# Kernel optimization log

Hardware: AMD Instinct MI355X
Metric: run time of the kernel (lower is better)

Reference implementation:

```python
import jax, jax.numpy as jnp
import numpy as np

D = 512
H_MAX = 32
W_MAX = 32
BATCH = 16


def _embeds_1d(L: int, d: int) -> jnp.ndarray:
    # Faithful to torch _embeds_1d: denom = L ** (2*cumsum(ones)/d) = L**(2*(j+1)/d)
    # (numer broadcast interpreted as per-position arange over rows, the intended math)
    numer = jnp.arange(L, dtype=jnp.float32)[:, None]            # [L,1]
    exps = 2.0 * jnp.arange(1, d + 1, dtype=jnp.float32) / d     # [d]
    denom = jnp.float32(L) ** exps                               # [d]
    e = numer / denom                                            # [L,d]
    return jnp.zeros_like(e).at[:, 0::2].set(jnp.sin(e[:, 0::2])).at[:, 1::2].set(jnp.cos(e[:, 1::2]))


def make_embed(H: int, W: int, d: int) -> jnp.ndarray:
    # [H,W,d] = embed_h[:,None,:] + embed_w[None,:,:]
    return _embeds_1d(H, d)[:, None, :] + _embeds_1d(W, d)[None, :, :]


def setup_inputs() -> dict:
    key = jax.random.key(0)
    k1, k2 = jax.random.split(key)
    q = jax.random.normal(k1, (BATCH, H_MAX, W_MAX, D), dtype=jnp.float32)
    k = jax.random.normal(k2, (BATCH, H_MAX, W_MAX, D), dtype=jnp.float32)
    embed = make_embed(H_MAX, W_MAX, D)
    return {"q": q, "k": k, "embed": embed}


def reference(q, k, embed):
    # content->position logits + position->(content+position) logits
    # q: [b,i,j,d], k: [b,k,l,d], embed: [i,j,d] (= q_embed = k_embed)
    logits = (jnp.einsum('bijd,kld->bijkl', q, embed)
              + jnp.einsum('ijd,bkld->bijkl', embed, k + embed))
    return logits  # [b,i,j,k,l]
```

## Files before the change

### kernel.cpp

```cpp
#include <hip/hip_runtime.h>
#include <stdint.h>

#define DD 512
#define NP 1024
#define NB 16

typedef __attribute__((ext_vector_type(8))) __bf16 bf16x8;
typedef __attribute__((ext_vector_type(4))) float f32x4;

__global__ __launch_bounds__(256) void thin_gemm(
    const float* __restrict__ q, const float* __restrict__ kin,
    const float* __restrict__ embed,
    float* __restrict__ qhw, float* __restrict__ khw)
{
    __shared__ __align__(16) unsigned short EHW[64 * 512];

    const int tid  = threadIdx.x;
    const int lane = tid & 63;
    const int wid  = tid >> 6;

    #pragma unroll
    for (int it = 0; it < 16; ++it) {
        int flat = it * 2048 + tid * 8;
        int row = flat >> 9, col = flat & 511;
        int srcrow = (row < 32) ? (row << 5) : (row - 32);
        const float* sp = embed + (size_t)srcrow * DD + col;
        float4 a = *(const float4*)sp;
        float4 c = *(const float4*)(sp + 4);
        if (row >= 32) {
            float4 z0 = *(const float4*)(embed + col);
            float4 z1 = *(const float4*)(embed + col + 4);
            a.x -= z0.x; a.y -= z0.y; a.z -= z0.z; a.w -= z0.w;
            c.x -= z1.x; c.y -= z1.y; c.z -= z1.z; c.w -= z1.w;
        }
        bf16x8 r;
        r[0] = (__bf16)a.x; r[1] = (__bf16)a.y; r[2] = (__bf16)a.z; r[3] = (__bf16)a.w;
        r[4] = (__bf16)c.x; r[5] = (__bf16)c.y; r[6] = (__bf16)c.z; r[7] = (__bf16)c.w;
        int byte = (col * 2) ^ ((row & 7) << 4);
        *(bf16x8*)((char*)EHW + row * 1024 + byte) = r;
    }
    __syncthreads();

    const int g2 = (blockIdx.x >= 256) ? 1 : 0;
    const int lr = lane & 15;
    const int kq = (lane >> 4) * 8;

    const float* srcA;
    const float* srcE = nullptr;
    if (!g2) {
        srcA = q + (size_t)(blockIdx.x * 64 + wid * 16 + lr) * DD;
    } else {
        int idx = blockIdx.x - 256;
        int b = idx >> 4, qt = idx & 15;
        int Qrow = qt * 64 + wid * 16 + lr;
        srcA = kin + ((size_t)b * NP + Qrow) * DD;
        srcE = embed + (size_t)Qrow * DD;
    }

    f32x4 acc[4];
    #pragma unroll
    for (int n = 0; n < 4; ++n) acc[n] = (f32x4)0.0f;

    #pragma unroll 4
    for (int kk = 0; kk < DD; kk += 32) {
        float4 a0 = *(const float4*)(srcA + kk + kq);
        float4 a1 = *(const float4*)(srcA + kk + kq + 4);
        if (g2) {
            float4 e0 = *(const float4*)(srcE + kk + kq);
            float4 e1 = *(const float4*)(srcE + kk + kq + 4);
            a0.x += e0.x; a0.y += e0.y; a0.z += e0.z; a0.w += e0.w;
            a1.x += e1.x; a1.y += e1.y; a1.z += e1.z; a1.w += e1.w;
        }
        bf16x8 sf;
        sf[0]=(__bf16)a0.x; sf[1]=(__bf16)a0.y; sf[2]=(__bf16)a0.z; sf[3]=(__bf16)a0.w;
        sf[4]=(__bf16)a1.x; sf[5]=(__bf16)a1.y; sf[6]=(__bf16)a1.z; sf[7]=(__bf16)a1.w;
        bf16x8 ef[4];
        #pragma unroll
        for (int n = 0; n < 4; ++n) {
            int row = n * 16 + lr;
            int byte = ((kk + kq) * 2) ^ ((row & 7) << 4);
            ef[n] = *(const bf16x8*)((const char*)EHW + row * 1024 + byte);
        }
        if (!g2) {
            #pragma unroll
            for (int n = 0; n < 4; ++n)
                acc[n] = __builtin_amdgcn_mfma_f32_16x16x32_bf16(sf, ef[n], acc[n], 0, 0, 0);
        } else {
            #pragma unroll
            for (int n = 0; n < 4; ++n)
                acc[n] = __builtin_amdgcn_mfma_f32_16x16x32_bf16(ef[n], sf, acc[n], 0, 0, 0);
        }
    }

    if (!g2) {
        float* o = qhw + (size_t)(blockIdx.x * 64 + wid * 16 + (lane >> 4) * 4) * 64;
        #pragma unroll
        for (int n = 0; n < 4; ++n)
            #pragma unroll
            for (int i = 0; i < 4; ++i)
                o[(size_t)i * 64 + n * 16 + lr] = acc[n][i];
    } else {
        int idx = blockIdx.x - 256;
        int b = idx >> 4, qt = idx & 15;
        float* o = khw + (size_t)b * 64 * NP + qt * 64 + wid * 16 + lr;
        #pragma unroll
        for (int n = 0; n < 4; ++n) {
            int m = n * 16 + (lane >> 4) * 4;
            #pragma unroll
            for (int i = 0; i < 4; ++i)
                o[(size_t)(m + i) * NP] = acc[n][i];
        }
    }
}

__global__ __launch_bounds__(256) void assemble(
    const float* __restrict__ qhw, const float* __restrict__ khw,
    float* __restrict__ out)
{
    __shared__ __align__(16) float kh[NP];
    __shared__ __align__(16) float qq[16 * 64];

    const int tid = threadIdx.x;
    const int b   = blockIdx.x >> 6;
    const int i   = (blockIdx.x >> 1) & 31;
    const int jh  = blockIdx.x & 1;

    ((float4*)kh)[tid] = ((const float4*)(khw + ((size_t)b * 64 + i) * NP))[tid];
    ((float4*)qq)[tid] =
        ((const float4*)(qhw + ((size_t)(b * NP + i * 32 + jh * 16)) * 64))[tid];
    __syncthreads();

    const int Q0 = tid * 4;
    const int kidx = Q0 >> 5;
    const int lidx = Q0 & 31;
    const float4 khv = *(const float4*)&kh[Q0];

    float* orow = out + ((size_t)(b * NP + i * 32 + jh * 16)) * NP + Q0;
    const float* kwbase = khw + ((size_t)b * 64 + 32 + jh * 16) * NP + Q0;

    #pragma unroll 4
    for (int jj = 0; jj < 16; ++jj) {
        float4 kw = *(const float4*)(kwbase + (size_t)jj * NP);
        float qh  = qq[jj * 64 + kidx];
        float4 qw = *(const float4*)&qq[jj * 64 + 32 + lidx];
        float4 v;
        v.x = khv.x + kw.x + qh + qw.x;
        v.y = khv.y + kw.y + qh + qw.y;
        v.z = khv.z + kw.z + qh + qw.z;
        v.w = khv.w + kw.w + qh + qw.w;
        *(float4*)(orow + (size_t)jj * NP) = v;
    }
}

extern "C" void kernel_launch(void* const* d_in, const int* in_sizes, int n_in,
                              void* d_out, int out_size, void* d_ws, size_t ws_size,
                              hipStream_t stream) {
    const float* q = (const float*)d_in[0];
    const float* k = (const float*)d_in[1];
    const float* e = (const float*)d_in[2];
    float* out = (float*)d_out;

    float* qhw = (float*)d_ws;
    float* khw = qhw + (size_t)NB * NP * 64;

    hipLaunchKernelGGL(thin_gemm, dim3(512), dim3(256), 0, stream, q, k, e, qhw, khw);
    hipLaunchKernelGGL(assemble, dim3(1024), dim3(256), 0, stream, qhw, khw, out);
}
```

Measured before the change: 50.62 us.

## Precompute bf16 embedding fragments once and split GEMM into smaller tiles

Moves the per-block conversion of the 64x512 rank embedding into bf16 LDS into a separate tiny prep kernel. That kernel writes the values to workspace in MFMA fragment order, which the GEMM then reads straight from global/L2. The GEMM grid doubles to 1024 blocks of 32 rows, with waves split across rows and the N dimension. This drops the 64KB LDS use, which should allow higher occupancy, and removes the redundant conversion done in every block. The cost is an extra kernel launch and reading embedding fragments from L2 instead of LDS.

```diff
diff --git a/kernel.cpp b/kernel.cpp
--- a/kernel.cpp
+++ b/kernel.cpp
@@ -8,108 +8,102 @@
 typedef __attribute__((ext_vector_type(8))) __bf16 bf16x8;
 typedef __attribute__((ext_vector_type(4))) float f32x4;
 
-__global__ __launch_bounds__(256) void thin_gemm(
+__global__ __launch_bounds__(256) void prep_ehwf(
+    const float* __restrict__ embed, unsigned short* __restrict__ ehwf)
+{
+    int g = blockIdx.x * 256 + threadIdx.x;
+    int c = g & 3;
+    int row = (g >> 2) & 63;
+    int ks = g >> 8;
+    int col = ks * 32 + c * 8;
+    int srcrow = (row < 32) ? (row << 5) : (row - 32);
+    const float* src = embed + (size_t)srcrow * DD + col;
+    float4 a = *(const float4*)src;
+    float4 d = *(const float4*)(src + 4);
+    if (row >= 32) {
+        float4 z0 = *(const float4*)(embed + col);
+        float4 z1 = *(const float4*)(embed + col + 4);
+        a.x -= z0.x; a.y -= z0.y; a.z -= z0.z; a.w -= z0.w;
+        d.x -= z1.x; d.y -= z1.y; d.z -= z1.z; d.w -= z1.w;
+    }
+    bf16x8 r;
+    r[0]=(__bf16)a.x; r[1]=(__bf16)a.y; r[2]=(__bf16)a.z; r[3]=(__bf16)a.w;
+    r[4]=(__bf16)d.x; r[5]=(__bf16)d.y; r[6]=(__bf16)d.z; r[7]=(__bf16)d.w;
+    *(bf16x8*)(ehwf + (size_t)g * 8) = r;
+}
+
+__global__ __launch_bounds__(256, 4) void rank_gemm(
     const float* __restrict__ q, const float* __restrict__ kin,
     const float* __restrict__ embed,
+    const unsigned short* __restrict__ ehwf,
     float* __restrict__ qhw, float* __restrict__ khw)
 {
-    __shared__ __align__(16) unsigned short EHW[64 * 512];
-
     const int tid  = threadIdx.x;
     const int lane = tid & 63;
     const int wid  = tid >> 6;
-
-    #pragma unroll
-    for (int it = 0; it < 16; ++it) {
-        int flat = it * 2048 + tid * 8;
-        int row = flat >> 9, col = flat & 511;
-        int srcrow = (row < 32) ? (row << 5) : (row - 32);
-        const float* sp = embed + (size_t)srcrow * DD + col;
-        float4 a = *(const float4*)sp;
-        float4 c = *(const float4*)(sp + 4);
-        if (row >= 32) {
-            float4 z0 = *(const float4*)(embed + col);
-            float4 z1 = *(const float4*)(embed + col + 4);
-            a.x -= z0.x; a.y -= z0.y; a.z -= z0.z; a.w -= z0.w;
-            c.x -= z1.x; c.y -= z1.y; c.z -= z1.z; c.w -= z1.w;
-        }
-        bf16x8 r;
-        r[0] = (__bf16)a.x; r[1] = (__bf16)a.y; r[2] = (__bf16)a.z; r[3] = (__bf16)a.w;
-        r[4] = (__bf16)c.x; r[5] = (__bf16)c.y; r[6] = (__bf16)c.z; r[7] = (__bf16)c.w;
-        int byte = (col * 2) ^ ((row & 7) << 4);
-        *(bf16x8*)((char*)EHW + row * 1024 + byte) = r;
-    }
-    __syncthreads();
-
-    const int g2 = (blockIdx.x >= 256) ? 1 : 0;
+    const int wa = wid >> 1;
+    const int wn = wid & 1;
     const int lr = lane & 15;
     const int kq = (lane >> 4) * 8;
 
+    const bool g2 = blockIdx.x >= 512;
     const float* srcA;
     const float* srcE = nullptr;
     if (!g2) {
-        srcA = q + (size_t)(blockIdx.x * 64 + wid * 16 + lr) * DD;
+        srcA = q + (size_t)(blockIdx.x * 32 + wa * 16 + lr) * DD + kq;
     } else {
-        int idx = blockIdx.x - 256;
-        int b = idx >> 4, qt = idx & 15;
-        int Qrow = qt * 64 + wid * 16 + lr;
-        srcA = kin + ((size_t)b * NP + Qrow) * DD;
-        srcE = embed + (size_t)Qrow * DD;
+        int gi = blockIdx.x - 512;
+        int b = gi >> 5, qt = gi & 31;
+        int Q = qt * 32 + wa * 16 + lr;
+        srcA = kin + ((size_t)b * NP + Q) * DD + kq;
+        srcE = embed + (size_t)Q * DD + kq;
     }
+    const unsigned short* tb =
+        ehwf + ((size_t)(wn * 32 + lr) * 4 + (lane >> 4)) * 8;
 
-    f32x4 acc[4];
-    #pragma unroll
-    for (int n = 0; n < 4; ++n) acc[n] = (f32x4)0.0f;
+    f32x4 acc0 = (f32x4)0.0f, acc1 = (f32x4)0.0f;
 
     #pragma unroll 4
-    for (int kk = 0; kk < DD; kk += 32) {
-        float4 a0 = *(const float4*)(srcA + kk + kq);
-        float4 a1 = *(const float4*)(srcA + kk + kq + 4);
+    for (int ks = 0; ks < 16; ++ks) {
+        float4 a0 = *(const float4*)(srcA + ks * 32);
+        float4 a1 = *(const float4*)(srcA + ks * 32 + 4);
         if (g2) {
-            float4 e0 = *(const float4*)(srcE + kk + kq);
-            float4 e1 = *(const float4*)(srcE + kk + kq + 4);
+            float4 e0 = *(const float4*)(srcE + ks * 32);
+            float4 e1 = *(const float4*)(srcE + ks * 32 + 4);
             a0.x += e0.x; a0.y += e0.y; a0.z += e0.z; a0.w += e0.w;
             a1.x += e1.x; a1.y += e1.y; a1.z += e1.z; a1.w += e1.w;
         }
         bf16x8 sf;
         sf[0]=(__bf16)a0.x; sf[1]=(__bf16)a0.y; sf[2]=(__bf16)a0.z; sf[3]=(__bf16)a0.w;
         sf[4]=(__bf16)a1.x; sf[5]=(__bf16)a1.y; sf[6]=(__bf16)a1.z; sf[7]=(__bf16)a1.w;
-        bf16x8 ef[4];
-        #pragma unroll
-        for (int n = 0; n < 4; ++n) {
-            int row = n * 16 + lr;
-            int byte = ((kk + kq) * 2) ^ ((row & 7) << 4);
-            ef[n] = *(const bf16x8*)((const char*)EHW + row * 1024 + byte);
-        }
+        bf16x8 ef0 = *(const bf16x8*)(tb + (size_t)ks * 2048);
+        bf16x8 ef1 = *(const bf16x8*)(tb + (size_t)ks * 2048 + 512);
         if (!g2) {
-            #pragma unroll
-            for (int n = 0; n < 4; ++n)
-                acc[n] = __builtin_amdgcn_mfma_f32_16x16x32_bf16(sf, ef[n], acc[n], 0, 0, 0);
+            acc0 = __builtin_amdgcn_mfma_f32_16x16x32_bf16(sf, ef0, acc0, 0, 0, 0);
+            acc1 = __builtin_amdgcn_mfma_f32_16x16x32_bf16(sf, ef1, acc1, 0, 0, 0);
         } else {
-            #pragma unroll
-            for (int n = 0; n < 4; ++n)
-                acc[n] = __builtin_amdgcn_mfma_f32_16x16x32_bf16(ef[n], sf, acc[n], 0, 0, 0);
+            acc0 = __builtin_amdgcn_mfma_f32_16x16x32_bf16(ef0, sf, acc0, 0, 0, 0);
+            acc1 = __builtin_amdgcn_mfma_f32_16x16x32_bf16(ef1, sf, acc1, 0, 0, 0);
         }
     }
 
     if (!g2) {
-        float* o = qhw + (size_t)(blockIdx.x * 64 + wid * 16 + (lane >> 4) * 4) * 64;
+        float* o = qhw + (size_t)(blockIdx.x * 32 + wa * 16 + (lane >> 4) * 4) * 64
+                       + wn * 32 + lr;
         #pragma unroll
-        for (int n = 0; n < 4; ++n)
-            #pragma unroll
-            for (int i = 0; i < 4; ++i)
-                o[(size_t)i * 64 + n * 16 + lr] = acc[n][i];
+        for (int i = 0; i < 4; ++i) o[(size_t)i * 64]      = acc0[i];
+        #pragma unroll
+        for (int i = 0; i < 4; ++i) o[(size_t)i * 64 + 16] = acc1[i];
     } else {
-        int idx = blockIdx.x - 256;
-        int b = idx >> 4, qt = idx & 15;
-        float* o = khw + (size_t)b * 64 * NP + qt * 64 + wid * 16 + lr;
+        int gi = blockIdx.x - 512;
+        int b = gi >> 5, qt = gi & 31;
+        int Q = qt * 32 + wa * 16 + lr;
+        float* o = khw + (size_t)b * 64 * NP + Q;
+        int m0 = wn * 32 + (lane >> 4) * 4;
         #pragma unroll
-        for (int n = 0; n < 4; ++n) {
-            int m = n * 16 + (lane >> 4) * 4;
-            #pragma unroll
-            for (int i = 0; i < 4; ++i)
-                o[(size_t)(m + i) * NP] = acc[n][i];
-        }
+        for (int i = 0; i < 4; ++i) o[(size_t)(m0 + i) * NP]      = acc0[i];
+        #pragma unroll
+        for (int i = 0; i < 4; ++i) o[(size_t)(m0 + 16 + i) * NP] = acc1[i];
     }
 }
 
@@ -162,7 +156,10 @@
 
     float* qhw = (float*)d_ws;
     float* khw = qhw + (size_t)NB * NP * 64;
+    unsigned short* ehwf = (unsigned short*)(khw + (size_t)NB * 64 * NP);
 
-    hipLaunchKernelGGL(thin_gemm, dim3(512), dim3(256), 0, stream, q, k, e, qhw, khw);
+    hipLaunchKernelGGL(prep_ehwf, dim3(16), dim3(256), 0, stream, e, ehwf);
+    hipLaunchKernelGGL(rank_gemm, dim3(1024), dim3(256), 0, stream,
+                       q, k, e, ehwf, qhw, khw);
     hipLaunchKernelGGL(assemble, dim3(1024), dim3(256), 0, stream, qhw, khw, out);
 }
```

Measured after the change: 66.94 us. 1.32x slower.

## Precompute bf16 embed table and embed Gram, split-K the thin GEMM

Applied to the files above, without the earlier changes.

Adds a prep kernel that builds the swizzled bf16 embed-basis table once and computes the embed-embed Gram matrix G. This removes the per-block table construction and the per-element embed addition on the k side. The thin GEMM is split into two K halves with twice the blocks and stages the table into LDS via global_load_lds. The assemble kernel sums the partial halves and adds G terms. This adds a third launch and extra partial-sum reads in assemble in exchange for less redundant table work and more parallelism in the GEMM.

```diff
diff --git a/kernel.cpp b/kernel.cpp
--- a/kernel.cpp
+++ b/kernel.cpp
@@ -8,80 +8,123 @@
 typedef __attribute__((ext_vector_type(8))) __bf16 bf16x8;
 typedef __attribute__((ext_vector_type(4))) float f32x4;
 
-__global__ __launch_bounds__(256) void thin_gemm(
+#define QHW_HALF 1048576
+#define KHW_HALF 1048576
+
+__device__ __forceinline__ bf16x8 cvt8(const float4& a, const float4& b) {
+    bf16x8 r;
+    r[0]=(__bf16)a.x; r[1]=(__bf16)a.y; r[2]=(__bf16)a.z; r[3]=(__bf16)a.w;
+    r[4]=(__bf16)b.x; r[5]=(__bf16)b.y; r[6]=(__bf16)b.z; r[7]=(__bf16)b.w;
+    return r;
+}
+
+__device__ __forceinline__ bf16x8 ehw_row(const float* __restrict__ embed, int r,
+                                          int col, const float4& z0, const float4& z1) {
+    int srcrow = (r < 32) ? (r << 5) : (r - 32);
+    const float* sp = embed + (size_t)srcrow * DD + col;
+    float4 a = *(const float4*)sp;
+    float4 b = *(const float4*)(sp + 4);
+    if (r >= 32) {
+        a.x -= z0.x; a.y -= z0.y; a.z -= z0.z; a.w -= z0.w;
+        b.x -= z1.x; b.y -= z1.y; b.z -= z1.z; b.w -= z1.w;
+    }
+    return cvt8(a, b);
+}
+
+__global__ __launch_bounds__(256) void prep(
+    const float* __restrict__ embed, unsigned short* __restrict__ tbl,
+    float* __restrict__ G)
+{
+    const int tid = threadIdx.x;
+    if (blockIdx.x < 16) {
+        int g = blockIdx.x * 256 + tid;
+        int row = g >> 6;
+        int c8  = (g & 63) * 8;
+        float4 z0 = *(const float4*)(embed + c8);
+        float4 z1 = *(const float4*)(embed + c8 + 4);
+        bf16x8 r = ehw_row(embed, row, c8, z0, z1);
+        int h  = c8 >> 8;
+        int cl = c8 & 255;
+        int byte = (cl * 2) ^ ((row & 7) << 4);
+        *(bf16x8*)((char*)tbl + h * 32768 + row * 512 + byte) = r;
+    } else {
+        const int lane = tid & 63, wid = tid >> 6;
+        const int lr = lane & 15, kq = (lane >> 4) * 8;
+        f32x4 acc[4];
+        #pragma unroll
+        for (int n = 0; n < 4; ++n) acc[n] = (f32x4)0.0f;
+        for (int ks = 0; ks < 16; ++ks) {
+            int col = ks * 32 + kq;
+            float4 z0 = *(const float4*)(embed + col);
+            float4 z1 = *(const float4*)(embed + col + 4);
+            bf16x8 af = ehw_row(embed, wid * 16 + lr, col, z0, z1);
+            #pragma unroll
+            for (int n = 0; n < 4; ++n) {
+                bf16x8 bf = ehw_row(embed, n * 16 + lr, col, z0, z1);
+                acc[n] = __builtin_amdgcn_mfma_f32_16x16x32_bf16(af, bf, acc[n], 0, 0, 0);
+            }
+        }
+        int row0 = wid * 16 + (lane >> 4) * 4;
+        #pragma unroll
+        for (int n = 0; n < 4; ++n)
+            #pragma unroll
+            for (int i = 0; i < 4; ++i)
+                G[(size_t)(row0 + i) * 64 + n * 16 + lr] = acc[n][i];
+    }
+}
+
+__device__ __forceinline__ void gload_lds16(const void* g, void* l) {
+    __builtin_amdgcn_global_load_lds(
+        (const __attribute__((address_space(1))) unsigned int*)g,
+        (__attribute__((address_space(3))) unsigned int*)l,
+        16, 0, 0);
+}
+
+__global__ __launch_bounds__(256) void rank_gemm(
     const float* __restrict__ q, const float* __restrict__ kin,
-    const float* __restrict__ embed,
+    const unsigned short* __restrict__ tbl,
     float* __restrict__ qhw, float* __restrict__ khw)
 {
-    __shared__ __align__(16) unsigned short EHW[64 * 512];
+    __shared__ __align__(16) unsigned short T[64 * 256];
 
     const int tid  = threadIdx.x;
     const int lane = tid & 63;
     const int wid  = tid >> 6;
-
-    #pragma unroll
-    for (int it = 0; it < 16; ++it) {
-        int flat = it * 2048 + tid * 8;
-        int row = flat >> 9, col = flat & 511;
-        int srcrow = (row < 32) ? (row << 5) : (row - 32);
-        const float* sp = embed + (size_t)srcrow * DD + col;
-        float4 a = *(const float4*)sp;
-        float4 c = *(const float4*)(sp + 4);
-        if (row >= 32) {
-            float4 z0 = *(const float4*)(embed + col);
-            float4 z1 = *(const float4*)(embed + col + 4);
-            a.x -= z0.x; a.y -= z0.y; a.z -= z0.z; a.w -= z0.w;
-            c.x -= z1.x; c.y -= z1.y; c.z -= z1.z; c.w -= z1.w;
-        }
-        bf16x8 r;
-        r[0] = (__bf16)a.x; r[1] = (__bf16)a.y; r[2] = (__bf16)a.z; r[3] = (__bf16)a.w;
-        r[4] = (__bf16)c.x; r[5] = (__bf16)c.y; r[6] = (__bf16)c.z; r[7] = (__bf16)c.w;
-        int byte = (col * 2) ^ ((row & 7) << 4);
-        *(bf16x8*)((char*)EHW + row * 1024 + byte) = r;
-    }
-    __syncthreads();
-
-    const int g2 = (blockIdx.x >= 256) ? 1 : 0;
+    const int gsel  = blockIdx.x >> 9;
+    const int khalf = (blockIdx.x >> 8) & 1;
+    const int tile  = blockIdx.x & 255;
     const int lr = lane & 15;
     const int kq = (lane >> 4) * 8;
 
-    const float* srcA;
-    const float* srcE = nullptr;
-    if (!g2) {
-        srcA = q + (size_t)(blockIdx.x * 64 + wid * 16 + lr) * DD;
-    } else {
-        int idx = blockIdx.x - 256;
-        int b = idx >> 4, qt = idx & 15;
-        int Qrow = qt * 64 + wid * 16 + lr;
-        srcA = kin + ((size_t)b * NP + Qrow) * DD;
-        srcE = embed + (size_t)Qrow * DD;
-    }
+    const char* src = (const char*)tbl + khalf * 32768;
+    #pragma unroll
+    for (int c = 0; c < 8; ++c) {
+        int off = wid * 8192 + c * 1024;
+        gload_lds16(src + off + lane * 16, (char*)T + off);
+    }
+
+    const int grow = tile * 64 + wid * 16 + lr;
+    const float* srcA = (gsel ? kin : q) + (size_t)grow * DD + khalf * 256 + kq;
 
     f32x4 acc[4];
     #pragma unroll
     for (int n = 0; n < 4; ++n) acc[n] = (f32x4)0.0f;
 
+    __syncthreads();
+
     #pragma unroll 4
-    for (int kk = 0; kk < DD; kk += 32) {
-        float4 a0 = *(const float4*)(srcA + kk + kq);
-        float4 a1 = *(const float4*)(srcA + kk + kq + 4);
-        if (g2) {
-            float4 e0 = *(const float4*)(srcE + kk + kq);
-            float4 e1 = *(const float4*)(srcE + kk + kq + 4);
-            a0.x += e0.x; a0.y += e0.y; a0.z += e0.z; a0.w += e0.w;
-            a1.x += e1.x; a1.y += e1.y; a1.z += e1.z; a1.w += e1.w;
-        }
-        bf16x8 sf;
-        sf[0]=(__bf16)a0.x; sf[1]=(__bf16)a0.y; sf[2]=(__bf16)a0.z; sf[3]=(__bf16)a0.w;
-        sf[4]=(__bf16)a1.x; sf[5]=(__bf16)a1.y; sf[6]=(__bf16)a1.z; sf[7]=(__bf16)a1.w;
+    for (int ks = 0; ks < 8; ++ks) {
+        float4 a0 = *(const float4*)(srcA + ks * 32);
+        float4 a1 = *(const float4*)(srcA + ks * 32 + 4);
+        bf16x8 sf = cvt8(a0, a1);
         bf16x8 ef[4];
         #pragma unroll
         for (int n = 0; n < 4; ++n) {
             int row = n * 16 + lr;
-            int byte = ((kk + kq) * 2) ^ ((row & 7) << 4);
-            ef[n] = *(const bf16x8*)((const char*)EHW + row * 1024 + byte);
+            int byte = ((ks * 32 + kq) * 2) ^ ((row & 7) << 4);
+            ef[n] = *(const bf16x8*)((const char*)T + row * 512 + byte);
         }
-        if (!g2) {
+        if (!gsel) {
             #pragma unroll
             for (int n = 0; n < 4; ++n)
                 acc[n] = __builtin_amdgcn_mfma_f32_16x16x32_bf16(sf, ef[n], acc[n], 0, 0, 0);
@@ -92,42 +135,59 @@
         }
     }
 
-    if (!g2) {
-        float* o = qhw + (size_t)(blockIdx.x * 64 + wid * 16 + (lane >> 4) * 4) * 64;
+    if (!gsel) {
+        float* o = qhw + (size_t)khalf * QHW_HALF
+                 + (size_t)(tile * 64 + wid * 16 + (lane >> 4) * 4) * 64 + lr;
         #pragma unroll
         for (int n = 0; n < 4; ++n)
             #pragma unroll
             for (int i = 0; i < 4; ++i)
-                o[(size_t)i * 64 + n * 16 + lr] = acc[n][i];
+                o[(size_t)i * 64 + n * 16] = acc[n][i];
     } else {
-        int idx = blockIdx.x - 256;
-        int b = idx >> 4, qt = idx & 15;
-        float* o = khw + (size_t)b * 64 * NP + qt * 64 + wid * 16 + lr;
-        #pragma unroll
-        for (int n = 0; n < 4; ++n) {
-            int m = n * 16 + (lane >> 4) * 4;
+        int b = grow >> 10, Q = grow & 1023;
+        float* o = khw + (size_t)khalf * KHW_HALF + (size_t)b * 65536 + Q;
+        int m0 = (lane >> 4) * 4;
+        #pragma unroll
+        for (int n = 0; n < 4; ++n)
             #pragma unroll
             for (int i = 0; i < 4; ++i)
-                o[(size_t)(m + i) * NP] = acc[n][i];
-        }
+                o[(size_t)(n * 16 + m0 + i) * 1024] = acc[n][i];
     }
 }
 
 __global__ __launch_bounds__(256) void assemble(
     const float* __restrict__ qhw, const float* __restrict__ khw,
-    float* __restrict__ out)
+    const float* __restrict__ G, float* __restrict__ out)
 {
     __shared__ __align__(16) float kh[NP];
-    __shared__ __align__(16) float qq[16 * 64];
+    __shared__ __align__(16) float d1[16][32];
+    __shared__ __align__(16) float d2[16][32];
 
     const int tid = threadIdx.x;
     const int b   = blockIdx.x >> 6;
     const int i   = (blockIdx.x >> 1) & 31;
     const int jh  = blockIdx.x & 1;
 
-    ((float4*)kh)[tid] = ((const float4*)(khw + ((size_t)b * 64 + i) * NP))[tid];
-    ((float4*)qq)[tid] =
-        ((const float4*)(qhw + ((size_t)(b * NP + i * 32 + jh * 16)) * 64))[tid];
+    const float* khA = khw + (size_t)b * 65536 + (size_t)i * 1024;
+    const float* khB = khA + KHW_HALF;
+    float4 ka = ((const float4*)khA)[tid];
+    float4 kb = ((const float4*)khB)[tid];
+    float4 ks; ks.x = ka.x + kb.x; ks.y = ka.y + kb.y; ks.z = ka.z + kb.z; ks.w = ka.w + kb.w;
+    ((float4*)kh)[tid] = ks;
+
+    {
+        int jj = tid >> 4, c = tid & 15;
+        int j  = jh * 16 + jj;
+        size_t Prow = (size_t)b * NP + i * 32 + j;
+        const float* qA = qhw + Prow * 64;
+        const float* qB = qA + QHW_HALF;
+        const float* Gi = G + (size_t)i * 64;
+        const float* Gj = G + (size_t)(32 + j) * 64;
+        d1[jj][c]      = qA[c]      + qB[c]      + Gi[c]      + Gj[c];
+        d1[jj][c + 16] = qA[c + 16] + qB[c + 16] + Gi[c + 16] + Gj[c + 16];
+        d2[jj][c]      = qA[32 + c]      + qB[32 + c]      + Gi[32 + c]      + Gj[32 + c];
+        d2[jj][c + 16] = qA[48 + c] + qB[48 + c] + Gi[48 + c] + Gj[48 + c];
+    }
     __syncthreads();
 
     const int Q0 = tid * 4;
@@ -135,19 +195,21 @@
     const int lidx = Q0 & 31;
     const float4 khv = *(const float4*)&kh[Q0];
 
-    float* orow = out + ((size_t)(b * NP + i * 32 + jh * 16)) * NP + Q0;
-    const float* kwbase = khw + ((size_t)b * 64 + 32 + jh * 16) * NP + Q0;
+    float* orow = out + ((size_t)b * NP + i * 32 + jh * 16) * NP + Q0;
+    const float* kwA = khw + (size_t)b * 65536 + (size_t)(32 + jh * 16) * 1024 + Q0;
+    const float* kwB = kwA + KHW_HALF;
 
     #pragma unroll 4
     for (int jj = 0; jj < 16; ++jj) {
-        float4 kw = *(const float4*)(kwbase + (size_t)jj * NP);
-        float qh  = qq[jj * 64 + kidx];
-        float4 qw = *(const float4*)&qq[jj * 64 + 32 + lidx];
+        float4 ka2 = *(const float4*)(kwA + (size_t)jj * 1024);
+        float4 kb2 = *(const float4*)(kwB + (size_t)jj * 1024);
+        float  s1  = d1[jj][kidx];
+        float4 s2  = *(const float4*)&d2[jj][lidx];
         float4 v;
-        v.x = khv.x + kw.x + qh + qw.x;
-        v.y = khv.y + kw.y + qh + qw.y;
-        v.z = khv.z + kw.z + qh + qw.z;
-        v.w = khv.w + kw.w + qh + qw.w;
+        v.x = khv.x + ka2.x + kb2.x + s1 + s2.x;
+        v.y = khv.y + ka2.y + kb2.y + s1 + s2.y;
+        v.z = khv.z + ka2.z + kb2.z + s1 + s2.z;
+        v.w = khv.w + ka2.w + kb2.w + s1 + s2.w;
         *(float4*)(orow + (size_t)jj * NP) = v;
     }
 }
@@ -161,8 +223,11 @@
     float* out = (float*)d_out;
 
     float* qhw = (float*)d_ws;
-    float* khw = qhw + (size_t)NB * NP * 64;
-
-    hipLaunchKernelGGL(thin_gemm, dim3(512), dim3(256), 0, stream, q, k, e, qhw, khw);
-    hipLaunchKernelGGL(assemble, dim3(1024), dim3(256), 0, stream, qhw, khw, out);
-}
+    float* khw = qhw + 2 * (size_t)QHW_HALF;
+    unsigned short* tbl = (unsigned short*)(khw + 2 * (size_t)KHW_HALF);
+    float* G = (float*)((char*)tbl + 65536);
+
+    hipLaunchKernelGGL(prep, dim3(17), dim3(256), 0, stream, e, tbl, G);
+    hipLaunchKernelGGL(rank_gemm, dim3(1024), dim3(256), 0, stream, q, k, tbl, qhw, khw);
+    hipLaunchKernelGGL(assemble, dim3(1024), dim3(256), 0, stream, qhw, khw, G, out);
+}
```

Result: slower. 69.36 us (+37.0%).
